# Kernel optimization log

Measured on AMD Instinct MI355X. Metric: run time of the kernel, lower is better.

Reference implementation:

```python
import jax, jax.numpy as jnp
import numpy as np

B, T, HID = 1, 2048, 2048
H, KVH, D = 32, 8, 64
G = H // KVH          # kv groups = 4
SCALE = 1.0 / np.sqrt(D)
NEG = -1e9


def _rotate_half(x):
    x1, x2 = x[..., : D // 2], x[..., D // 2 :]
    return jnp.concatenate((-x2, x1), axis=-1)


def setup_inputs() -> dict:
    key = jax.random.key(0)
    ks = jax.random.split(key, 8)
    hidden_states = jax.random.normal(ks[0], (B, T, HID), jnp.float32)
    # RoPE tables (faithful shapes; realistic values)
    pos = jnp.arange(T, dtype=jnp.float32)[:, None]
    inv = 1.0 / (10000.0 ** (jnp.arange(0, D, 2, dtype=jnp.float32) / D))
    ang = pos * inv[None, :]                      # [T, D/2]
    ang = jnp.concatenate([ang, ang], axis=-1)    # [T, D]
    cos = jnp.broadcast_to(jnp.cos(ang)[None], (B, T, D))
    sin = jnp.broadcast_to(jnp.sin(ang)[None], (B, T, D))
    # causal additive mask [B,1,T,T]
    causal = jnp.tril(jnp.ones((T, T), bool))
    attention_mask_4d = jnp.where(causal, 0.0, NEG).astype(jnp.float32)[None, None]
    s = 0.02
    Wq = jax.random.normal(ks[1], (H * D, HID), jnp.float32) * s
    Wk = jax.random.normal(ks[2], (KVH * D, HID), jnp.float32) * s
    Wv = jax.random.normal(ks[3], (KVH * D, HID), jnp.float32) * s
    Wo = jax.random.normal(ks[4], (HID, H * D), jnp.float32) * s
    return {"hidden_states": hidden_states, "cos": cos, "sin": sin,
            "attention_mask_4d": attention_mask_4d,
            "Wq": Wq, "Wk": Wk, "Wv": Wv, "Wo": Wo}


def reference(hidden_states, cos, sin, attention_mask_4d, Wq, Wk, Wv, Wo):
    x = hidden_states
    b, t, _ = x.shape
    # QKV projections (nn.Linear: x @ W.T), then [B, heads, T, D]
    q = (x @ Wq.T).reshape(b, t, H, D).transpose(0, 2, 1, 3)
    k = (x @ Wk.T).reshape(b, t, KVH, D).transpose(0, 2, 1, 3)
    v = (x @ Wv.T).reshape(b, t, KVH, D).transpose(0, 2, 1, 3)
    # rotary: cos/sin [B,T,D] -> broadcast over heads
    c = cos[:, None]; s = sin[:, None]
    q = q * c + _rotate_half(q) * s
    k = k * c + _rotate_half(k) * s
    # grouped-query attention with fp32 scores/softmax
    qg = q.reshape(b, KVH, G, t, D)
    scores = jnp.einsum('bkgtd,bksd->bkgts', qg.astype(jnp.float32),
                        k.astype(jnp.float32)) * SCALE
    m = attention_mask_4d[:, 0].astype(jnp.float32)  # [B,T,S]
    scores = scores + m[:, None, None, :, :]
    probs = jax.nn.softmax(scores, axis=-1)
    out = jnp.einsum('bkgts,bksd->bkgtd', probs.astype(v.dtype), v)
    out = out.astype(q.dtype).reshape(b, H, t, D)
    out = out.transpose(0, 2, 1, 3).reshape(b, t, H * D)
    return out @ Wo.T
```

## Files before the change

kernel.cpp:

```cpp
#include <hip/hip_runtime.h>
#include <math.h>

typedef __attribute__((ext_vector_type(8))) __bf16 bf16x8;
typedef __attribute__((ext_vector_type(4))) float  f32x4;
typedef unsigned short ushort_t;
typedef unsigned int   uint_t;

static __device__ inline f32x4 mfma16(bf16x8 a, bf16x8 b, f32x4 c) {
    return __builtin_amdgcn_mfma_f32_16x16x32_bf16(a, b, c, 0, 0, 0);
}

static __device__ inline ushort_t f2b(float f) {
    uint_t u = __builtin_bit_cast(uint_t, f);
    u = (u + 0x7FFFu + ((u >> 16) & 1u)) >> 16;
    return (ushort_t)u;
}
static __device__ inline float b2f(ushort_t u) {
    uint_t x = ((uint_t)u) << 16;
    return __builtin_bit_cast(float, x);
}
static __device__ inline bf16x8 ld8(const ushort_t* p) {
    uint4 v = *(const uint4*)p;
    return __builtin_bit_cast(bf16x8, v);
}
static __device__ inline float fexp2(float x) {
#if __has_builtin(__builtin_amdgcn_exp2f)
    return __builtin_amdgcn_exp2f(x);
#else
    return exp2f(x);
#endif
}

static __device__ inline void gl_lds16(const ushort_t* g, ushort_t* l) {
    __builtin_amdgcn_global_load_lds(
        (const __attribute__((address_space(1))) void*)(g),
        (__attribute__((address_space(3))) void*)(l),
        16, 0, 0);
}

#define WS_XB     0
#define WS_WQKV   8388608
#define WS_WO     20971520
#define WS_P0     29360128
#define WS_P1     41943040
#define WS_QBB    0
#define WS_KBB    8388608
#define WS_VTG    10485760
#define WS_AB     12582912

__global__ __launch_bounds__(256) void cvt_all(const float* __restrict__ x,
                                               const float* __restrict__ wq,
                                               const float* __restrict__ wk,
                                               const float* __restrict__ wv,
                                               const float* __restrict__ wo,
                                               ushort_t* __restrict__ dst) {
    const size_t i = (size_t)(blockIdx.x * 256 + threadIdx.x) * 4;
    const float* src; size_t off;
    if (i < 4194304)       { src = x;  off = 0; }
    else if (i < 8388608)  { src = wq; off = 4194304; }
    else if (i < 9437184)  { src = wk; off = 8388608; }
    else if (i < 10485760) { src = wv; off = 9437184; }
    else                   { src = wo; off = 10485760; }
    float4 v = *(const float4*)(src + (i - off));
    ushort4 o;
    o.x = f2b(v.x); o.y = f2b(v.y); o.z = f2b(v.z); o.w = f2b(v.w);
    *(ushort4*)(dst + i) = o;
}

template <int OUTB>
__global__ __launch_bounds__(512, 2) void gemm256(const ushort_t* __restrict__ A,
                                                  const ushort_t* __restrict__ Bt,
                                                  void* __restrict__ C0,
                                                  void* __restrict__ C1,
                                                  int N, int K) {
    __shared__ ushort_t lds[65536];
    const int tid  = threadIdx.x;
    const int lane = tid & 63, w = tid >> 6;
    const int qn = lane & 15, quad = lane >> 4;
    const long m0 = (long)blockIdx.y * 256;
    const long n0 = (long)blockIdx.x * 256;
    const int kh   = K >> 1;
    const int kbeg = blockIdx.z * kh;
    const int NT   = kh >> 6;
    void* Cout = blockIdx.z ? C1 : C0;
    ushort_t* ldsp = lds;

    const int srow = w * 8 + (lane >> 3);
    const int scol = ((lane & 7) ^ (lane >> 3)) * 8;
    const ushort_t* gA = A  + (m0 + srow) * (size_t)K + kbeg + scol;
    const ushort_t* gB = Bt + (n0 + srow) * (size_t)K + kbeg + scol;

    const int aRow = ((w >> 2) * 64 + qn) * 64;
    const int bRow = ((w & 3) * 32 + qn) * 64;
    const int sw0 = ((quad * 16)      ^ ((qn & 7) << 4)) >> 1;
    const int sw1 = ((64 + quad * 16) ^ ((qn & 7) << 4)) >> 1;

#define STG_A(t, h, buf)                                                       \
    do { if ((t) < NT) {                                                       \
        const ushort_t* g = gA + (size_t)(h) * 128 * K + (t) * 64;             \
        ushort_t* d = ldsp + (buf) * 32768 + (h) * 8192 + w * 512;             \
        gl_lds16(g, d);                                                        \
        gl_lds16(g + 64 * (size_t)K, d + 4096);                                \
    } } while (0)
#define STG_B(t, h, buf)                                                       \
    do { if ((t) < NT) {                                                       \
        const ushort_t* g = gB + (size_t)(h) * 128 * K + (t) * 64;             \
        ushort_t* d = ldsp + (buf) * 32768 + 16384 + (h) * 8192 + w * 512;     \
        gl_lds16(g, d);                                                        \
        gl_lds16(g + 64 * (size_t)K, d + 4096);                                \
    } } while (0)

#define PHASE(cb, p, qr, qc, STAGE, BOUND)                                     \
    do {                                                                       \
        const ushort_t* bA = ldsp + (cb) * 32768 + (qr) * 8192;                \
        const ushort_t* bB = ldsp + (cb) * 32768 + 16384 + (qc) * 8192;        \
        bf16x8 af[4][2], bv[2][2];                                             \
        _Pragma("unroll")                                                      \
        for (int mi = 0; mi < 4; mi++) {                                       \
            af[mi][0] = *(const bf16x8*)(bA + aRow + mi * 1024 + sw0);         \
            af[mi][1] = *(const bf16x8*)(bA + aRow + mi * 1024 + sw1);         \
        }                                                                      \
        _Pragma("unroll")                                                      \
        for (int nj = 0; nj < 2; nj++) {                                       \
            bv[nj][0] = *(const bf16x8*)(bB + bRow + nj * 1024 + sw0);         \
            bv[nj][1] = *(const bf16x8*)(bB + bRow + nj * 1024 + sw1);         \
        }                                                                      \
        asm volatile("" ::: "memory");          \
        STAGE;                                                                 \
        BOUND;                                                                 \
        __builtin_amdgcn_s_barrier();                                          \
        asm volatile("s_waitcnt lgkmcnt(0)" ::: "memory");                     \
        __builtin_amdgcn_sched_barrier(0);                                     \
        __builtin_amdgcn_s_setprio(1);                                         \
        _Pragma("unroll")                                                      \
        for (int mi = 0; mi < 4; mi++)                                         \
            _Pragma("unroll")                                                  \
            for (int nj = 0; nj < 2; nj++) {                                   \
                acc[p][mi][nj] = mfma16(af[mi][0], bv[nj][0], acc[p][mi][nj]); \
                acc[p][mi][nj] = mfma16(af[mi][1], bv[nj][1], acc[p][mi][nj]); \
            }                                                                  \
        __builtin_amdgcn_s_setprio(0);                                         \
        __builtin_amdgcn_s_barrier();                                          \
    } while (0)

    f32x4 acc[4][4][2];
    f32x4 zero = {0.f, 0.f, 0.f, 0.f};
    #pragma unroll
    for (int p = 0; p < 4; p++)
        #pragma unroll
        for (int mi = 0; mi < 4; mi++)
            #pragma unroll
            for (int nj = 0; nj < 2; nj++) acc[p][mi][nj] = zero;

    STG_A(0, 0, 0); STG_B(0, 0, 0); STG_B(0, 1, 0); STG_A(0, 1, 0);
    STG_A(1, 0, 1); STG_B(1, 0, 1);
    asm volatile("s_waitcnt vmcnt(0)" ::: "memory");
    __builtin_amdgcn_s_barrier();

    for (int t2 = 0; t2 < NT; t2 += 2) {
        PHASE(0, 0, 0, 0, STG_B(t2 + 1, 1, 1), (void)0);
        PHASE(0, 1, 0, 1, STG_A(t2 + 1, 1, 1), (void)0);
        PHASE(0, 2, 1, 0, STG_A(t2 + 2, 0, 0), (void)0);
        PHASE(0, 3, 1, 1, STG_B(t2 + 2, 0, 0),
              if (t2 == NT - 2) { asm volatile("s_waitcnt vmcnt(0)" ::: "memory"); }
              else              { asm volatile("s_waitcnt vmcnt(4)" ::: "memory"); });
        PHASE(1, 0, 0, 0, STG_B(t2 + 2, 1, 0), (void)0);
        PHASE(1, 1, 0, 1, STG_A(t2 + 2, 1, 0), (void)0);
        PHASE(1, 2, 1, 0, STG_A(t2 + 3, 0, 1), (void)0);
        PHASE(1, 3, 1, 1, STG_B(t2 + 3, 0, 1),
              asm volatile("s_waitcnt vmcnt(4)" ::: "memory"););
    }
#undef PHASE
#undef STG_A
#undef STG_B

    #pragma unroll
    for (int p = 0; p < 4; p++) {
        const int qr = p >> 1, qc = p & 1;
        #pragma unroll
        for (int mi = 0; mi < 4; mi++)
            #pragma unroll
            for (int nj = 0; nj < 2; nj++) {
                const long row0 = m0 + qr * 128 + (w >> 2) * 64 + mi * 16 + quad * 4;
                const long col  = n0 + qc * 128 + (w & 3) * 32 + nj * 16 + qn;
                #pragma unroll
                for (int r = 0; r < 4; r++) {
                    if (OUTB)
                        ((ushort_t*)Cout)[(row0 + r) * N + col] = f2b(acc[p][mi][nj][r]);
                    else
                        ((float*)Cout)[(row0 + r) * N + col] = acc[p][mi][nj][r];
                }
            }
    }
}

__global__ __launch_bounds__(512, 2) void gemm_on(const ushort_t* __restrict__ A,
                                                  const ushort_t* __restrict__ Bt,
                                                  float* __restrict__ Cout,
                                                  int N, int K) {
    __shared__ ushort_t lds[40960];
    const int tid  = threadIdx.x;
    const int lane = tid & 63, w = tid >> 6;
    const int qn = lane & 15, quad = lane >> 4;
    const long m0 = (long)blockIdx.y * 256;
    const long n0 = (long)blockIdx.x * 64;
    const int NT = K >> 6;
    ushort_t* ldsp = lds;

    const int srow = w * 8 + (lane >> 3);
    const int scol = ((lane & 7) ^ (lane >> 3)) * 8;
    const ushort_t* gA = A + (m0 + srow) * (size_t)K + scol;
    const int srB  = tid >> 3;
    const int scB  = ((tid & 7) ^ (srB & 7)) * 8;
    const ushort_t* gB = Bt + (n0 + srB) * (size_t)K + scB;

    const int wm = w >> 1, wn = w & 1;
    const int aRow = (wm * 32 + qn) * 64;
    const int bRow = (wn * 32 + qn) * 64;
    const int sw0 = ((quad * 16)      ^ ((qn & 7) << 4)) >> 1;
    const int sw1 = ((64 + quad * 16) ^ ((qn & 7) << 4)) >> 1;

#define NSTG_A(t, h, buf)                                                      \
    do { if ((t) < NT) {                                                       \
        const ushort_t* g = gA + (size_t)(h) * 128 * K + (t) * 64;             \
        ushort_t* d = ldsp + (buf) * 20480 + (h) * 8192 + w * 512;             \
        gl_lds16(g, d);                                                        \
        gl_lds16(g + 64 * (size_t)K, d + 4096);                                \
    } } while (0)
#define NSTG_B(t, buf)                                                         \
    do { if ((t) < NT) {                                                       \
        const ushort_t* g = gB + (size_t)(t) * 64;                             \
        ushort_t* d = ldsp + (buf) * 20480 + 16384 + w * 512;                  \
        gl_lds16(g, d);                                                        \
    } } while (0)

#define NPHASE(cb, qr, STAGE, BOUND)                                           \
    do {                                                                       \
        const ushort_t* bA = ldsp + (cb) * 20480 + (qr) * 8192;                \
        const ushort_t* bB = ldsp + (cb) * 20480 + 16384;                      \
        bf16x8 af[2][2], bv[2][2];                                             \
        _Pragma("unroll")                                                      \
        for (int mi = 0; mi < 2; mi++) {                                       \
            af[mi][0] = *(const bf16x8*)(bA + aRow + mi * 1024 + sw0);         \
            af[mi][1] = *(const bf16x8*)(bA + aRow + mi * 1024 + sw1);         \
        }                                                                      \
        _Pragma("unroll")                                                      \
        for (int nj = 0; nj < 2; nj++) {                                       \
            bv[nj][0] = *(const bf16x8*)(bB + bRow + nj * 1024 + sw0);         \
            bv[nj][1] = *(const bf16x8*)(bB + bRow + nj * 1024 + sw1);         \
        }                                                                      \
        asm volatile("" ::: "memory");                                         \
        STAGE;                                                                 \
        BOUND;                                                                 \
        __builtin_amdgcn_s_barrier();                                          \
        asm volatile("s_waitcnt lgkmcnt(0)" ::: "memory");                     \
        __builtin_amdgcn_sched_barrier(0);                                     \
        __builtin_amdgcn_s_setprio(1);                                         \
        _Pragma("unroll")                                                      \
        for (int mi = 0; mi < 2; mi++)                                         \
            _Pragma("unroll")                                                  \
            for (int nj = 0; nj < 2; nj++) {                                   \
                acc[qr][mi][nj] = mfma16(af[mi][0], bv[nj][0], acc[qr][mi][nj]); \
                acc[qr][mi][nj] = mfma16(af[mi][1], bv[nj][1], acc[qr][mi][nj]); \
            }                                                                  \
        __builtin_amdgcn_s_setprio(0);                                         \
        __builtin_amdgcn_s_barrier();                                          \
    } while (0)

    f32x4 acc[2][2][2];
    f32x4 zero = {0.f, 0.f, 0.f, 0.f};
    #pragma unroll
    for (int p = 0; p < 2; p++)
        #pragma unroll
        for (int mi = 0; mi < 2; mi++)
            #pragma unroll
            for (int nj = 0; nj < 2; nj++) acc[p][mi][nj] = zero;

    NSTG_A(0, 0, 0); NSTG_A(0, 1, 0); NSTG_B(0, 0);
    NSTG_A(1, 0, 1);
    asm volatile("s_waitcnt vmcnt(0)" ::: "memory");
    __builtin_amdgcn_s_barrier();

    for (int t = 0; t < NT; t++) {
        const int cb = t & 1;
        NPHASE(cb, 0, { NSTG_A(t + 1, 1, cb ^ 1); NSTG_B(t + 1, cb ^ 1); },
               (void)0);
        NPHASE(cb, 1, { NSTG_A(t + 2, 0, cb); },
               if (t == NT - 2) { asm volatile("s_waitcnt vmcnt(0)" ::: "memory"); }
               else             { asm volatile("s_waitcnt vmcnt(2)" ::: "memory"); });
    }
#undef NPHASE
#undef NSTG_A
#undef NSTG_B

    #pragma unroll
    for (int p = 0; p < 2; p++)
        #pragma unroll
        for (int mi = 0; mi < 2; mi++)
            #pragma unroll
            for (int nj = 0; nj < 2; nj++) {
                const long row0 = m0 + p * 128 + wm * 32 + mi * 16 + quad * 4;
                const long col  = n0 + wn * 32 + nj * 16 + qn;
                #pragma unroll
                for (int r = 0; r < 4; r++)
                    Cout[(row0 + r) * N + col] = acc[p][mi][nj][r];
            }
}

__global__ __launch_bounds__(256) void fuse_crv(const ushort_t* __restrict__ p0,
                                                const ushort_t* __restrict__ p1,
                                                const float* __restrict__ cs,
                                                const float* __restrict__ sn,
                                                ushort_t* __restrict__ qd,
                                                ushort_t* __restrict__ kd,
                                                ushort_t* __restrict__ vt) {
    __shared__ ushort_t tl[64][65];
    const int cx = blockIdx.x;
    const int ty = blockIdx.y;
    const int r  = threadIdx.x >> 2;
    const int c0 = (threadIdx.x & 3) << 4;
    const int t  = ty * 64 + r;
    const size_t base = (size_t)t * 3072 + cx * 64;

    if (cx < 40) {
        const int cp = c0 ^ 32;
        float own[16], par[16];
        #pragma unroll
        for (int jj = 0; jj < 2; jj++) {
            uint4 a = *(const uint4*)(p0 + base + c0 + jj * 8);
            uint4 b = *(const uint4*)(p1 + base + c0 + jj * 8);
            uint4 c = *(const uint4*)(p0 + base + cp + jj * 8);
            uint4 d = *(const uint4*)(p1 + base + cp + jj * 8);
            const ushort_t* pa = (const ushort_t*)&a;
            const ushort_t* pb = (const ushort_t*)&b;
            const ushort_t* pc = (const ushort_t*)&c;
            const ushort_t* pd = (const ushort_t*)&d;
            #pragma unroll
            for (int e = 0; e < 8; e++) {
                own[jj * 8 + e] = b2f(pa[e]) + b2f(pb[e]);
                par[jj * 8 + e] = b2f(pc[e]) + b2f(pd[e]);
            }
        }
        float cs16[16], sn16[16];
        #pragma unroll
        for (int jj = 0; jj < 4; jj++) {
            float4 c4 = *(const float4*)(cs + (size_t)t * 64 + c0 + jj * 4);
            float4 s4 = *(const float4*)(sn + (size_t)t * 64 + c0 + jj * 4);
            cs16[jj * 4 + 0] = c4.x; cs16[jj * 4 + 1] = c4.y;
            cs16[jj * 4 + 2] = c4.z; cs16[jj * 4 + 3] = c4.w;
            sn16[jj * 4 + 0] = s4.x; sn16[jj * 4 + 1] = s4.y;
            sn16[jj * 4 + 2] = s4.z; sn16[jj * 4 + 3] = s4.w;
        }
        const float scale = (cx < 32) ? 0.18033688f : 1.0f;
        union { ushort_t u[16]; uint4 v[2]; } o;
        #pragma unroll
        for (int j = 0; j < 16; j++) {
            const int d = c0 + j;
            const float pr = (d < 32) ? -par[j] : par[j];
            o.u[j] = f2b((own[j] * cs16[j] + pr * sn16[j]) * scale);
        }
        if (cx < 32) {
            ushort_t* dst = qd + (size_t)t * 2048 + cx * 64 + c0;
            *(uint4*)dst = o.v[0]; *(uint4*)(dst + 8) = o.v[1];
        } else {
            ushort_t* dst = kd + (size_t)t * 512 + (cx - 32) * 64 + c0;
            *(uint4*)dst = o.v[0]; *(uint4*)(dst + 8) = o.v[1];
        }
    } else {
        #pragma unroll
        for (int jj = 0; jj < 2; jj++) {
            uint4 a = *(const uint4*)(p0 + base + c0 + jj * 8);
            uint4 b = *(const uint4*)(p1 + base + c0 + jj * 8);
            const ushort_t* pa = (const ushort_t*)&a;
            const ushort_t* pb = (const ushort_t*)&b;
            #pragma unroll
            for (int e = 0; e < 8; e++)
                tl[r][c0 + jj * 8 + e] = f2b(b2f(pa[e]) + b2f(pb[e]));
        }
        __syncthreads();
        const int rr  = threadIdx.x >> 3;
        const int cc8 = (threadIdx.x & 7) * 8;
        const int db = (cx - 40) * 64, tb = ty * 64;
        #pragma unroll
        for (int h = 0; h < 2; h++) {
            const int d = rr + h * 32;
            ushort4 o0, o1;
            o0.x = tl[cc8 + 0][d]; o0.y = tl[cc8 + 1][d];
            o0.z = tl[cc8 + 2][d]; o0.w = tl[cc8 + 3][d];
            o1.x = tl[cc8 + 4][d]; o1.y = tl[cc8 + 5][d];
            o1.z = tl[cc8 + 6][d]; o1.w = tl[cc8 + 7][d];
            *(ushort4*)(vt + (size_t)(db + d) * 2048 + tb + cc8)     = o0;
            *(ushort4*)(vt + (size_t)(db + d) * 2048 + tb + cc8 + 4) = o1;
        }
    }
}

__global__ __launch_bounds__(256) void attn_kernel(const ushort_t* __restrict__ Q,
                                                   const ushort_t* __restrict__ Kb,
                                                   const ushort_t* __restrict__ Vt,
                                                   ushort_t* __restrict__ Ob) {
    __shared__ ushort_t Ks[2 * 4096];
    __shared__ ushort_t Vs[2 * 4096];
    __shared__ ushort_t pl[4 * 16 * 72];
    const int tid  = threadIdx.x;
    const int lane = tid & 63, wid = tid >> 6;
    const int qn = lane & 15, quad = lane >> 4;
    const int h   = blockIdx.x & 31;
    const int qb  = 31 - (blockIdx.x >> 5);
    const int kvb = (h >> 2) * 64;
    const int trow = qb * 64 + wid * 16;
    ushort_t* plw = pl + wid * 16 * 72;
    f32x4 zero = {0.f, 0.f, 0.f, 0.f};

    const ushort_t* qpA = Q + (size_t)(trow + qn) * 2048 + h * 64 + quad * 8;
    const bf16x8 qA0 = ld8(qpA), qA1 = ld8(qpA + 32);

    f32x4 oA[4] = {zero, zero, zero, zero};
    float lsum = 0.f;
    const int ntiles = qb + 1;

#define STAGE(s0, buf)                                                         \
    do {                                                                       \
        const ushort_t* kg = Kb + (size_t)((s0) + lane) * 512 + kvb + wid * 8; \
        gl_lds16(kg,      Ks + (buf) * 4096 + wid * 512);                      \
        gl_lds16(kg + 32, Ks + (buf) * 4096 + (wid + 4) * 512);                \
        const ushort_t* vg = Vt + (size_t)(kvb + lane) * 2048 + (s0) + wid * 8;\
        gl_lds16(vg,      Vs + (buf) * 4096 + wid * 512);                      \
        gl_lds16(vg + 32, Vs + (buf) * 4096 + (wid + 4) * 512);                \
    } while (0)

#define COMPUTE(s0, buf)                                                       \
    do {                                                                       \
        f32x4 scA[4];                                                          \
        __builtin_amdgcn_s_setprio(1);                                         \
        _Pragma("unroll")                                                      \
        for (int cb = 0; cb < 4; cb++) {                                       \
            const bf16x8 kf0 = *(const bf16x8*)(Ks + (buf) * 4096 + quad * 512 + (cb * 16 + qn) * 8);       \
            const bf16x8 kf1 = *(const bf16x8*)(Ks + (buf) * 4096 + (quad + 4) * 512 + (cb * 16 + qn) * 8); \
            f32x4 s = mfma16(kf0, qA0, zero); scA[cb] = mfma16(kf1, qA1, s);   \
        }                                                                      \
        __builtin_amdgcn_s_setprio(0);                                         \
        const bool needmask = ((s0) + 63 > trow);                              \
        const int tA = trow + qn;                                              \
        _Pragma("unroll")                                                      \
        for (int cb = 0; cb < 4; cb++) {                                       \
            float pv0, pv1, pv2, pv3;                                          \
            {                                                                  \
                const int colb = (s0) + cb * 16 + quad * 4;                    \
                float v0 = scA[cb][0], v1 = scA[cb][1];                        \
                float v2 = scA[cb][2], v3 = scA[cb][3];                        \
                if (needmask) {                                                \
                    if (colb + 0 > tA) v0 = -INFINITY;                         \
                    if (colb + 1 > tA) v1 = -INFINITY;                         \
                    if (colb + 2 > tA) v2 = -INFINITY;                         \
                    if (colb + 3 > tA) v3 = -INFINITY;                         \
                }                                                              \
                pv0 = fexp2(v0); pv1 = fexp2(v1);                              \
                pv2 = fexp2(v2); pv3 = fexp2(v3);                              \
            }                                                                  \
            lsum += pv0 + pv1 + pv2 + pv3;                                     \
            uint_t w0, w1;                                                     \
            asm("v_cvt_pk_bf16_f32 %0, %1, %2" : "=v"(w0) : "v"(pv0), "v"(pv1)); \
            asm("v_cvt_pk_bf16_f32 %0, %1, %2" : "=v"(w1) : "v"(pv2), "v"(pv3)); \
            uint2 pk; pk.x = w0; pk.y = w1;                                    \
            *(uint2*)(plw + qn * 72 + cb * 16 + quad * 4) = pk;                \
        }                                                                      \
        const bf16x8 pfA0 = *(const bf16x8*)(plw + qn * 72 + quad * 8);        \
        const bf16x8 pfA1 = *(const bf16x8*)(plw + qn * 72 + 32 + quad * 8);   \
        __builtin_amdgcn_s_setprio(1);                                         \
        _Pragma("unroll")                                                      \
        for (int dcb = 0; dcb < 4; dcb++) {                                    \
            const bf16x8 vf0 = *(const bf16x8*)(Vs + (buf) * 4096 + quad * 512 + (dcb * 16 + qn) * 8);       \
            const bf16x8 vf1 = *(const bf16x8*)(Vs + (buf) * 4096 + (quad + 4) * 512 + (dcb * 16 + qn) * 8); \
            oA[dcb] = mfma16(pfA0, vf0, oA[dcb]);                              \
            oA[dcb] = mfma16(pfA1, vf1, oA[dcb]);                              \
        }                                                                      \
        __builtin_amdgcn_s_setprio(0);                                         \
    } while (0)

    STAGE(0, 0);
    int t = 0;
    for (; t + 2 <= ntiles; t += 2) {
        __syncthreads();
        STAGE((t + 1) * 64, 1);
        COMPUTE(t * 64, 0);
        __syncthreads();
        if (t + 2 < ntiles) STAGE((t + 2) * 64, 0);
        COMPUTE((t + 1) * 64, 1);
    }
    if (t < ntiles) {
        __syncthreads();
        COMPUTE(t * 64, 0);
    }
#undef STAGE
#undef COMPUTE

    float sA = lsum;
    sA += __shfl_xor(sA, 16, 64);
    sA += __shfl_xor(sA, 32, 64);
    #pragma unroll
    for (int i = 0; i < 4; i++) {
        const float invA = 1.0f / __shfl(sA, quad * 4 + i, 64);
        ushort_t* obA = Ob + (size_t)(trow + quad * 4 + i) * 2048 + h * 64 + qn;
        obA[0]  = f2b(oA[0][i] * invA);
        obA[16] = f2b(oA[1][i] * invA);
        obA[32] = f2b(oA[2][i] * invA);
        obA[48] = f2b(oA[3][i] * invA);
    }
}

extern "C" void kernel_launch(void* const* d_in, const int* in_sizes, int n_in,
                              void* d_out, int out_size, void* d_ws, size_t ws_size,
                              hipStream_t stream) {
    const float* x    = (const float*)d_in[0];
    const float* cosp = (const float*)d_in[1];
    const float* sinp = (const float*)d_in[2];
    const float* Wq = (const float*)d_in[4];
    const float* Wk = (const float*)d_in[5];
    const float* Wv = (const float*)d_in[6];
    const float* Wo = (const float*)d_in[7];
    char* ws = (char*)d_ws;
    (void)ws_size; (void)in_sizes; (void)n_in; (void)out_size;

    ushort_t* xb    = (ushort_t*)(ws + WS_XB);
    ushort_t* wqkvb = (ushort_t*)(ws + WS_WQKV);
    ushort_t* wob   = (ushort_t*)(ws + WS_WO);
    ushort_t* p0    = (ushort_t*)(ws + WS_P0);
    ushort_t* p1    = (ushort_t*)(ws + WS_P1);
    ushort_t* qbb   = (ushort_t*)(ws + WS_QBB);
    ushort_t* kbb   = (ushort_t*)(ws + WS_KBB);
    ushort_t* vtg   = (ushort_t*)(ws + WS_VTG);
    ushort_t* ab    = (ushort_t*)(ws + WS_AB);

    cvt_all<<<14336, 256, 0, stream>>>(x, Wq, Wk, Wv, Wo, xb);

    gemm256<1><<<dim3(12, 8, 2), 512, 0, stream>>>(xb, wqkvb, p0, p1, 3072, 2048);

    fuse_crv<<<dim3(48, 32), 256, 0, stream>>>(p0, p1, cosp, sinp, qbb, kbb, vtg);

    attn_kernel<<<1024, 256, 0, stream>>>(qbb, kbb, vtg, ab);

    gemm_on<<<dim3(32, 8), 512, 0, stream>>>(ab, wob, (float*)d_out, 2048, 2048);
}
```

Baseline: 238.0 us.

## Replace split-K QKV GEMM with full-K 256x128 tiles and single partial output

The QKV projection GEMM drops its 2-way split-K, which wrote two bf16 partial buffers that the RoPE/V-transpose kernel then summed. It now runs full K per block with a 256x128 output tile, keeping the same 192-block grid, and writes one bf16 result. The fuse kernel reads a single buffer and skips the add. This removes a partial-buffer write and read and one bf16 rounding step. In exchange each block runs twice as many K iterations with a smaller per-wave tile, which lowers MFMA work per LDS load.

```diff
diff --git a/kernel.cpp b/kernel.cpp
--- a/kernel.cpp
+++ b/kernel.cpp
@@ -42,7 +42,6 @@
 #define WS_WQKV   8388608
 #define WS_WO     20971520
 #define WS_P0     29360128
-#define WS_P1     41943040
 #define WS_QBB    0
 #define WS_KBB    8388608
 #define WS_VTG    10485760
@@ -67,56 +66,53 @@
     *(ushort4*)(dst + i) = o;
 }
 
-template <int OUTB>
-__global__ __launch_bounds__(512, 2) void gemm256(const ushort_t* __restrict__ A,
+__global__ __launch_bounds__(512, 2) void gemm_fk(const ushort_t* __restrict__ A,
                                                   const ushort_t* __restrict__ Bt,
-                                                  void* __restrict__ C0,
-                                                  void* __restrict__ C1,
+                                                  ushort_t* __restrict__ Cout,
                                                   int N, int K) {
-    __shared__ ushort_t lds[65536];
+    __shared__ ushort_t lds[49152];
     const int tid  = threadIdx.x;
     const int lane = tid & 63, w = tid >> 6;
     const int qn = lane & 15, quad = lane >> 4;
     const long m0 = (long)blockIdx.y * 256;
-    const long n0 = (long)blockIdx.x * 256;
-    const int kh   = K >> 1;
-    const int kbeg = blockIdx.z * kh;
-    const int NT   = kh >> 6;
-    void* Cout = blockIdx.z ? C1 : C0;
+    const long n0 = (long)blockIdx.x * 128;
+    const int NT = K >> 6;
     ushort_t* ldsp = lds;
 
     const int srow = w * 8 + (lane >> 3);
     const int scol = ((lane & 7) ^ (lane >> 3)) * 8;
-    const ushort_t* gA = A  + (m0 + srow) * (size_t)K + kbeg + scol;
-    const ushort_t* gB = Bt + (n0 + srow) * (size_t)K + kbeg + scol;
-
-    const int aRow = ((w >> 2) * 64 + qn) * 64;
-    const int bRow = ((w & 3) * 32 + qn) * 64;
+    const ushort_t* gA = A + (m0 + srow) * (size_t)K + scol;
+    const int srB  = tid >> 3;
+    const int scB  = ((tid & 7) ^ (srB & 7)) * 8;
+    const ushort_t* gB = Bt + (n0 + srB) * (size_t)K + scB;
+
+    const int wm = w >> 1, wn = w & 1;
+    const int aRow = (wm * 32 + qn) * 64;
+    const int bRow = (wn * 32 + qn) * 64;
     const int sw0 = ((quad * 16)      ^ ((qn & 7) << 4)) >> 1;
     const int sw1 = ((64 + quad * 16) ^ ((qn & 7) << 4)) >> 1;
 
-#define STG_A(t, h, buf)                                                       \
+#define KSTG_A(t, h, buf)                                                      \
     do { if ((t) < NT) {                                                       \
         const ushort_t* g = gA + (size_t)(h) * 128 * K + (t) * 64;             \
-        ushort_t* d = ldsp + (buf) * 32768 + (h) * 8192 + w * 512;             \
+        ushort_t* d = ldsp + (buf) * 24576 + (h) * 8192 + w * 512;             \
         gl_lds16(g, d);                                                        \
         gl_lds16(g + 64 * (size_t)K, d + 4096);                                \
     } } while (0)
-#define STG_B(t, h, buf)                                                       \
+#define KSTG_B(t, h, buf)                                                      \
     do { if ((t) < NT) {                                                       \
-        const ushort_t* g = gB + (size_t)(h) * 128 * K + (t) * 64;             \
-        ushort_t* d = ldsp + (buf) * 32768 + 16384 + (h) * 8192 + w * 512;     \
+        const ushort_t* g = gB + (size_t)(h) * 64 * K + (t) * 64;              \
+        ushort_t* d = ldsp + (buf) * 24576 + 16384 + (h) * 4096 + w * 512;     \
         gl_lds16(g, d);                                                        \
-        gl_lds16(g + 64 * (size_t)K, d + 4096);                                \
     } } while (0)
 
-#define PHASE(cb, p, qr, qc, STAGE, BOUND)                                     \
+#define KPHASE(cb, p, qr, qc, STAGE, BOUND)                                    \
     do {                                                                       \
-        const ushort_t* bA = ldsp + (cb) * 32768 + (qr) * 8192;                \
-        const ushort_t* bB = ldsp + (cb) * 32768 + 16384 + (qc) * 8192;        \
-        bf16x8 af[4][2], bv[2][2];                                             \
-        _Pragma("unroll")                                                      \
-        for (int mi = 0; mi < 4; mi++) {                                       \
+        const ushort_t* bA = ldsp + (cb) * 24576 + (qr) * 8192;                \
+        const ushort_t* bB = ldsp + (cb) * 24576 + 16384 + (qc) * 4096;        \
+        bf16x8 af[2][2], bv[2][2];                                             \
+        _Pragma("unroll")                                                      \
+        for (int mi = 0; mi < 2; mi++) {                                       \
             af[mi][0] = *(const bf16x8*)(bA + aRow + mi * 1024 + sw0);         \
             af[mi][1] = *(const bf16x8*)(bA + aRow + mi * 1024 + sw1);         \
         }                                                                      \
@@ -125,7 +121,7 @@
             bv[nj][0] = *(const bf16x8*)(bB + bRow + nj * 1024 + sw0);         \
             bv[nj][1] = *(const bf16x8*)(bB + bRow + nj * 1024 + sw1);         \
         }                                                                      \
-        asm volatile("" ::: "memory");          \
+        asm volatile("" ::: "memory");                                         \
         STAGE;                                                                 \
         BOUND;                                                                 \
         __builtin_amdgcn_s_barrier();                                          \
@@ -133,7 +129,7 @@
         __builtin_amdgcn_sched_barrier(0);                                     \
         __builtin_amdgcn_s_setprio(1);                                         \
         _Pragma("unroll")                                                      \
-        for (int mi = 0; mi < 4; mi++)                                         \
+        for (int mi = 0; mi < 2; mi++)                                         \
             _Pragma("unroll")                                                  \
             for (int nj = 0; nj < 2; nj++) {                                   \
                 acc[p][mi][nj] = mfma16(af[mi][0], bv[nj][0], acc[p][mi][nj]); \
@@ -143,53 +139,49 @@
         __builtin_amdgcn_s_barrier();                                          \
     } while (0)
 
-    f32x4 acc[4][4][2];
+    f32x4 acc[4][2][2];
     f32x4 zero = {0.f, 0.f, 0.f, 0.f};
     #pragma unroll
     for (int p = 0; p < 4; p++)
         #pragma unroll
-        for (int mi = 0; mi < 4; mi++)
+        for (int mi = 0; mi < 2; mi++)
             #pragma unroll
             for (int nj = 0; nj < 2; nj++) acc[p][mi][nj] = zero;
 
-    STG_A(0, 0, 0); STG_B(0, 0, 0); STG_B(0, 1, 0); STG_A(0, 1, 0);
-    STG_A(1, 0, 1); STG_B(1, 0, 1);
+    KSTG_A(0, 0, 0); KSTG_B(0, 0, 0); KSTG_B(0, 1, 0); KSTG_A(0, 1, 0);
+    KSTG_A(1, 0, 1); KSTG_B(1, 0, 1);
     asm volatile("s_waitcnt vmcnt(0)" ::: "memory");
     __builtin_amdgcn_s_barrier();
 
     for (int t2 = 0; t2 < NT; t2 += 2) {
-        PHASE(0, 0, 0, 0, STG_B(t2 + 1, 1, 1), (void)0);
-        PHASE(0, 1, 0, 1, STG_A(t2 + 1, 1, 1), (void)0);
-        PHASE(0, 2, 1, 0, STG_A(t2 + 2, 0, 0), (void)0);
-        PHASE(0, 3, 1, 1, STG_B(t2 + 2, 0, 0),
-              if (t2 == NT - 2) { asm volatile("s_waitcnt vmcnt(0)" ::: "memory"); }
-              else              { asm volatile("s_waitcnt vmcnt(4)" ::: "memory"); });
-        PHASE(1, 0, 0, 0, STG_B(t2 + 2, 1, 0), (void)0);
-        PHASE(1, 1, 0, 1, STG_A(t2 + 2, 1, 0), (void)0);
-        PHASE(1, 2, 1, 0, STG_A(t2 + 3, 0, 1), (void)0);
-        PHASE(1, 3, 1, 1, STG_B(t2 + 3, 0, 1),
-              asm volatile("s_waitcnt vmcnt(4)" ::: "memory"););
-    }
-#undef PHASE
-#undef STG_A
-#undef STG_B
+        KPHASE(0, 0, 0, 0, KSTG_B(t2 + 1, 1, 1), (void)0);
+        KPHASE(0, 1, 0, 1, KSTG_A(t2 + 1, 1, 1), (void)0);
+        KPHASE(0, 2, 1, 0, KSTG_A(t2 + 2, 0, 0), (void)0);
+        KPHASE(0, 3, 1, 1, KSTG_B(t2 + 2, 0, 0),
+               if (t2 == NT - 2) { asm volatile("s_waitcnt vmcnt(0)" ::: "memory"); }
+               else              { asm volatile("s_waitcnt vmcnt(3)" ::: "memory"); });
+        KPHASE(1, 0, 0, 0, KSTG_B(t2 + 2, 1, 0), (void)0);
+        KPHASE(1, 1, 0, 1, KSTG_A(t2 + 2, 1, 0), (void)0);
+        KPHASE(1, 2, 1, 0, KSTG_A(t2 + 3, 0, 1), (void)0);
+        KPHASE(1, 3, 1, 1, KSTG_B(t2 + 3, 0, 1),
+               asm volatile("s_waitcnt vmcnt(3)" ::: "memory"););
+    }
+#undef KPHASE
+#undef KSTG_A
+#undef KSTG_B
 
     #pragma unroll
     for (int p = 0; p < 4; p++) {
         const int qr = p >> 1, qc = p & 1;
         #pragma unroll
-        for (int mi = 0; mi < 4; mi++)
+        for (int mi = 0; mi < 2; mi++)
             #pragma unroll
             for (int nj = 0; nj < 2; nj++) {
-                const long row0 = m0 + qr * 128 + (w >> 2) * 64 + mi * 16 + quad * 4;
-                const long col  = n0 + qc * 128 + (w & 3) * 32 + nj * 16 + qn;
+                const long row0 = m0 + qr * 128 + wm * 32 + mi * 16 + quad * 4;
+                const long col  = n0 + qc * 64 + wn * 32 + nj * 16 + qn;
                 #pragma unroll
-                for (int r = 0; r < 4; r++) {
-                    if (OUTB)
-                        ((ushort_t*)Cout)[(row0 + r) * N + col] = f2b(acc[p][mi][nj][r]);
-                    else
-                        ((float*)Cout)[(row0 + r) * N + col] = acc[p][mi][nj][r];
-                }
+                for (int r = 0; r < 4; r++)
+                    Cout[(row0 + r) * N + col] = f2b(acc[p][mi][nj][r]);
             }
     }
 }
@@ -308,7 +300,6 @@
 }
 
 __global__ __launch_bounds__(256) void fuse_crv(const ushort_t* __restrict__ p0,
-                                                const ushort_t* __restrict__ p1,
                                                 const float* __restrict__ cs,
                                                 const float* __restrict__ sn,
                                                 ushort_t* __restrict__ qd,
@@ -328,17 +319,13 @@
         #pragma unroll
         for (int jj = 0; jj < 2; jj++) {
             uint4 a = *(const uint4*)(p0 + base + c0 + jj * 8);
-            uint4 b = *(const uint4*)(p1 + base + c0 + jj * 8);
             uint4 c = *(const uint4*)(p0 + base + cp + jj * 8);
-            uint4 d = *(const uint4*)(p1 + base + cp + jj * 8);
             const ushort_t* pa = (const ushort_t*)&a;
-            const ushort_t* pb = (const ushort_t*)&b;
             const ushort_t* pc = (const ushort_t*)&c;
-            const ushort_t* pd = (const ushort_t*)&d;
             #pragma unroll
             for (int e = 0; e < 8; e++) {
-                own[jj * 8 + e] = b2f(pa[e]) + b2f(pb[e]);
-                par[jj * 8 + e] = b2f(pc[e]) + b2f(pd[e]);
+                own[jj * 8 + e] = b2f(pa[e]);
+                par[jj * 8 + e] = b2f(pc[e]);
             }
         }
         float cs16[16], sn16[16];
@@ -370,12 +357,10 @@
         #pragma unroll
         for (int jj = 0; jj < 2; jj++) {
             uint4 a = *(const uint4*)(p0 + base + c0 + jj * 8);
-            uint4 b = *(const uint4*)(p1 + base + c0 + jj * 8);
             const ushort_t* pa = (const ushort_t*)&a;
-            const ushort_t* pb = (const ushort_t*)&b;
             #pragma unroll
             for (int e = 0; e < 8; e++)
-                tl[r][c0 + jj * 8 + e] = f2b(b2f(pa[e]) + b2f(pb[e]));
+                tl[r][c0 + jj * 8 + e] = pa[e];
         }
         __syncthreads();
         const int rr  = threadIdx.x >> 3;
@@ -526,7 +511,6 @@
     ushort_t* wqkvb = (ushort_t*)(ws + WS_WQKV);
     ushort_t* wob   = (ushort_t*)(ws + WS_WO);
     ushort_t* p0    = (ushort_t*)(ws + WS_P0);
-    ushort_t* p1    = (ushort_t*)(ws + WS_P1);
     ushort_t* qbb   = (ushort_t*)(ws + WS_QBB);
     ushort_t* kbb   = (ushort_t*)(ws + WS_KBB);
     ushort_t* vtg   = (ushort_t*)(ws + WS_VTG);
@@ -534,9 +518,9 @@
 
     cvt_all<<<14336, 256, 0, stream>>>(x, Wq, Wk, Wv, Wo, xb);
 
-    gemm256<1><<<dim3(12, 8, 2), 512, 0, stream>>>(xb, wqkvb, p0, p1, 3072, 2048);
-
-    fuse_crv<<<dim3(48, 32), 256, 0, stream>>>(p0, p1, cosp, sinp, qbb, kbb, vtg);
+    gemm_fk<<<dim3(24, 8), 512, 0, stream>>>(xb, wqkvb, p0, 3072, 2048);
+
+    fuse_crv<<<dim3(48, 32), 256, 0, stream>>>(p0, cosp, sinp, qbb, kbb, vtg);
 
     attn_kernel<<<1024, 256, 0, stream>>>(qbb, kbb, vtg, ab);
 
```

Result: no change. 238.3 us (+0.1%).
